# Kernel tuning notes

Measured on AMD Instinct MI355X. Metric: run time of the kernel, lower is better.

Reference implementation:

```python
import jax, jax.numpy as jnp
import numpy as np

IMAGE_SIZE = 512
OUT_SIZE = 64
FEAT = 256
SCALES = [2.0, 4.0, 6.0]
RATIOS = [0.5, 1.0, 2.0]
POS_THR = 0.7
NEG_THR = 0.3
HW = OUT_SIZE - 2            # head grid after 3x3 VALID conv
A = len(SCALES) * len(RATIOS)
B, N = 16, 8


def _anchor_base():
    # mirrors get_anchor_base(out_size-2, ratios, scales): w=scale*ratio, h=scale,
    # centers at i+0.5, boxes [xmin,ymin,xmax,ymax] clipped to [0, HW]
    ctr = np.arange(HW, dtype=np.float32) + 0.5
    ws = np.array([s * r for r in RATIOS for s in SCALES], np.float32)
    hs = np.array([s for r in RATIOS for s in SCALES], np.float32)
    X = ctr[:, None, None]  # x index first, as in the torch loop
    Y = ctr[None, :, None]
    xmin = np.clip(X - ws / 2, 0, HW)
    xmax = np.clip(X + ws / 2, 0, HW)
    ymin = np.clip(Y - hs / 2, 0, HW)
    ymax = np.clip(Y + hs / 2, 0, HW)
    xmin, ymin, xmax, ymax = np.broadcast_arrays(xmin, ymin, xmax, ymax)
    return np.stack([xmin, ymin, xmax, ymax], -1).reshape(-1, 4)  # [T,4]


def _conv(x, w, b):
    y = jax.lax.conv_general_dilated(x, w, (1, 1), 'VALID',
                                     dimension_numbers=('NCHW', 'OIHW', 'NCHW'))
    return y + b[None, :, None, None]


def setup_inputs() -> dict:
    key = jax.random.key(0)
    ks = jax.random.split(key, 8)
    features = jax.random.normal(ks[0], (B, FEAT, OUT_SIZE, OUT_SIZE), jnp.float32)
    cxy = jax.random.uniform(ks[1], (B, N, 2), jnp.float32, 0.0, IMAGE_SIZE)
    half = jax.random.uniform(ks[2], (B, N, 2), jnp.float32, 10.0, 60.0)
    mins = jnp.clip(cxy - half, 0.0, IMAGE_SIZE)
    maxs = jnp.clip(cxy + half, 0.0, IMAGE_SIZE)
    gt_boxes = jnp.concatenate([mins, maxs], -1)  # [B,N,4] xyxy in image coords
    gt_class = jax.random.randint(ks[3], (B, N), 0, 21)
    conv_w = jax.random.normal(ks[4], (FEAT, FEAT, 3, 3), jnp.float32) * 0.02
    conv_b = jnp.zeros((FEAT,), jnp.float32)
    cls_w = jax.random.normal(ks[5], (A, FEAT, 1, 1), jnp.float32) * 0.02
    cls_b = jnp.zeros((A,), jnp.float32)
    box_w = jax.random.normal(ks[6], (4 * A, FEAT, 1, 1), jnp.float32) * 0.02
    box_b = jnp.zeros((4 * A,), jnp.float32)
    return dict(features=features, gt_boxes=gt_boxes, gt_class=gt_class,
                conv_w=conv_w, conv_b=conv_b, cls_w=cls_w, cls_b=cls_b,
                box_w=box_w, box_b=box_b)


def reference(features, gt_boxes, gt_class, conv_w, conv_b, cls_w, cls_b, box_w, box_b):
    b = features.shape[0]
    x = _conv(features, conv_w, conv_b)          # [B,FEAT,HW,HW]
    cls = _conv(x, cls_w, cls_b)                 # [B,A,HW,HW]
    bx = _conv(x, box_w, box_b)                  # [B,4A,HW,HW]
    cls = cls.transpose(0, 2, 3, 1).reshape(b, -1)                    # [B,T]
    pred_off = bx.transpose(0, 2, 3, 1).reshape(b, -1, 4)             # [B,T,4]

    anchors = jnp.asarray(_anchor_base())        # [T,4]
    scale = IMAGE_SIZE // HW
    gt = gt_boxes / scale                        # project_bboxes p2a

    ax1, ay1, ax2, ay2 = (anchors[:, i] for i in range(4))
    gx1, gy1, gx2, gy2 = (gt[..., i] for i in range(4))
    area_a = (ax2 - ax1) * (ay2 - ay1)                                 # [T]
    area_g = (gx2 - gx1) * (gy2 - gy1)                                 # [B,N]
    ix1 = jnp.maximum(ax1[None, :, None], gx1[:, None, :])
    iy1 = jnp.maximum(ay1[None, :, None], gy1[:, None, :])
    ix2 = jnp.minimum(ax2[None, :, None], gx2[:, None, :])
    iy2 = jnp.minimum(ay2[None, :, None], gy2[:, None, :])
    inter = jnp.clip(ix2 - ix1, 0) * jnp.clip(iy2 - iy1, 0)            # [B,T,N]
    union = area_a[None, :, None] + area_g[:, None, :] - inter
    iou = inter / jnp.maximum(union, 1e-9)                             # [B,T,N]

    max_per_gt = iou.max(axis=1, keepdims=True)                        # best anchor per GT
    pos_mask = ((iou == max_per_gt) & (max_per_gt > 0)) | (iou > POS_THR)
    posf = pos_mask.astype(jnp.float32)
    num_pos = jnp.maximum(posf.sum(), 1.0)

    # anchor / gt boxes in cxcywh
    acx, acy = (ax1 + ax2) / 2, (ay1 + ay2) / 2
    aw, ah = ax2 - ax1, ay2 - ay1
    gcx, gcy = (gx1 + gx2) / 2, (gy1 + gy2) / 2
    gw, gh = gx2 - gx1, gy2 - gy1
    # per (anchor, gt) pair offsets [B,T,N,4]
    tx = (gcx[:, None, :] - acx[None, :, None]) / aw[None, :, None]
    ty = (gcy[:, None, :] - acy[None, :, None]) / ah[None, :, None]
    tw = jnp.log(gw)[:, None, :] - jnp.log(aw)[None, :, None]
    th = jnp.log(gh)[:, None, :] - jnp.log(ah)[None, :, None]
    gt_off = jnp.stack([tx, ty, tw, th], -1)

    diff = pred_off[:, :, None, :] - gt_off
    ad = jnp.abs(diff)
    sl1 = jnp.where(ad < 1.0, 0.5 * diff * diff, ad - 0.5)
    reg_loss = (sl1 * posf[..., None]).sum() / (num_pos * 4.0)

    # BCE-with-logits: positives target 1, negatives (iou < neg_thr) target 0
    pos_loss = (jax.nn.softplus(-cls)[:, :, None] * posf).sum() / num_pos
    negf = (iou < NEG_THR).astype(jnp.float32)
    num_neg = jnp.maximum(negf.sum(), 1.0)
    neg_loss = (jax.nn.softplus(cls)[:, :, None] * negf).sum() / num_neg
    cls_loss = 0.5 * (pos_loss + neg_loss)

    # proposals from predicted offsets, all anchors (positives selectable via pos_mask)
    pcx = acx[None, :] + pred_off[..., 0] * aw[None, :]
    pcy = acy[None, :] + pred_off[..., 1] * ah[None, :]
    pw = aw[None, :] * jnp.exp(pred_off[..., 2])
    ph = ah[None, :] * jnp.exp(pred_off[..., 3])
    proposal_scale = OUT_SIZE / HW
    proposals = jnp.stack([pcx - pw / 2, pcy - ph / 2, pcx + pw / 2, pcy + ph / 2],
                          -1) * proposal_scale                          # [B,T,4]

    # class of best-matching GT per anchor (GT_pos_class analogue, full grid)
    best_gt = jnp.argmax(iou, axis=-1)                                  # [B,T]
    gt_cls_per_anchor = jnp.take_along_axis(
        jnp.broadcast_to(gt_class[:, None, :], iou.shape).astype(jnp.int32),
        best_gt[..., None].astype(jnp.int32), -1)[..., 0]

    return (cls_loss, reg_loss, proposals, pos_mask, gt_cls_per_anchor)
```

## Files before the change

### kernel.cpp

```cpp
#include <hip/hip_runtime.h>
#include <math.h>

#define HW2   62
#define NANCH 34596
#define NBAT  16
#define NGT   8
#define FEATC 256
#define NOUT  45
#define NBLK_C 496

typedef short bf16x8 __attribute__((ext_vector_type(8)));
typedef float f32x4  __attribute__((ext_vector_type(4)));
typedef float f32x2  __attribute__((ext_vector_type(2)));

#define AS1U(p) ((const __attribute__((address_space(1))) unsigned int*)(p))
#define AS3U(p) ((__attribute__((address_space(3))) unsigned int*)(p))

__device__ __forceinline__ unsigned short f2bf(float f) {
    unsigned int u = __float_as_uint(f);
    u = u + 0x7FFFu + ((u >> 16) & 1u);
    return (unsigned short)(u >> 16);
}


__device__ __forceinline__ void anchor4(int i, int j, int a,
                                        float& x1, float& y1, float& x2, float& y2) {
    int am = a % 3, ad = a / 3;
    float h = 2.f * (float)(am + 1);
    float w = h * 0.5f * (float)(1 << ad);
    float cx = (float)i + 0.5f, cy = (float)j + 0.5f;
    x1 = fminf(fmaxf(cx - 0.5f * w, 0.f), 62.f);
    x2 = fminf(fmaxf(cx + 0.5f * w, 0.f), 62.f);
    y1 = fminf(fmaxf(cy - 0.5f * h, 0.f), 62.f);
    y2 = fminf(fmaxf(cy + 0.5f * h, 0.f), 62.f);
}

__device__ __forceinline__ float iou_fn(float ax1, float ay1, float ax2, float ay2,
                                        float gx1, float gy1, float gx2, float gy2) {
    float area_a = __fmul_rn(__fsub_rn(ax2, ax1), __fsub_rn(ay2, ay1));
    float area_g = __fmul_rn(__fsub_rn(gx2, gx1), __fsub_rn(gy2, gy1));
    float ix1 = fmaxf(ax1, gx1), iy1 = fmaxf(ay1, gy1);
    float ix2 = fminf(ax2, gx2), iy2 = fminf(ay2, gy2);
    float iw = fmaxf(__fsub_rn(ix2, ix1), 0.f);
    float ih = fmaxf(__fsub_rn(iy2, iy1), 0.f);
    float inter = __fmul_rn(iw, ih);
    float uni = __fsub_rn(__fadd_rn(area_a, area_g), inter);
    return inter / fmaxf(uni, 1e-9f);
}

__device__ __forceinline__ float softplus_f(float x) {
    return fmaxf(x, 0.f) + log1pf(expf(-fabsf(x)));
}

__device__ __forceinline__ float sl1_f(float d) {
    float ad = fabsf(d);
    return (ad < 1.f) ? 0.5f * d * d : (ad - 0.5f);
}

__device__ __forceinline__ void to_bf16_body(const float* __restrict__ feat,
                                             unsigned short* __restrict__ ft,
                                             float* ldsT,
                                             int yp, int cc, int bz, int b, int t) {
    int y0 = yp * 2;
#pragma unroll
    for (int k = 0; k < 4; ++k) {
        int fi = k * 256 + t;
        int ch = fi >> 5, r = fi & 31;
        int y = r >> 4, xq = r & 15;
        f32x4 v = *(const f32x4*)(feat + ((size_t)(b * 256 + cc * 32 + ch) << 12)
                                  + (y0 + y) * 64 + xq * 4);
        int word = ch * 128 + y * 64 + ((xq * 4) ^ ((ch & 7) << 3));
        *(f32x4*)(ldsT + word) = v;
    }
    __syncthreads();
    int y = t >> 7, x = (t >> 1) & 63, h2 = t & 1;
    bf16x8 o0, o1;
#pragma unroll
    for (int j = 0; j < 8; ++j) {
        int ch = h2 * 16 + j;
        o0[j] = (short)f2bf(ldsT[ch * 128 + y * 64 + (x ^ ((ch & 7) << 3))]);
    }
#pragma unroll
    for (int j = 0; j < 8; ++j) {
        int ch = h2 * 16 + 8 + j;
        o1[j] = (short)f2bf(ldsT[ch * 128 + y * 64 + (x ^ ((ch & 7) << 3))]);
    }
    unsigned short* ftc = ft + ((size_t)(bz * 8 + cc) << 17);
    size_t p = (size_t)(y0 + y) * 64 + x;
    *(bf16x8*)(ftc + ((size_t)(h2 * 2) * 4096 + p) * 8) = o0;
    *(bf16x8*)(ftc + ((size_t)(h2 * 2 + 1) * 4096 + p) * 8) = o1;
}

__global__ void prep_all(const float* __restrict__ feat,
                         const float* __restrict__ conv_w,
                         const float* __restrict__ conv_b,
                         const float* __restrict__ cls_w,
                         const float* __restrict__ cls_b,
                         const float* __restrict__ box_w,
                         const float* __restrict__ box_b,
                         const float* __restrict__ gtb,
                         unsigned short* __restrict__ Bfrag,
                         float* __restrict__ effb,
                         float* __restrict__ maxiou,
                         unsigned short* __restrict__ ft) {
    __shared__ float ldsT[4096];
    __shared__ float red[256];
    int blk = blockIdx.x, t = threadIdx.x;
    if (blk < 432) {
        int i = blk * 256 + t;
        int o = i / 2304, idx = i - o * 2304;
        float s = 0.f;
        if (o < NOUT) {
            const float* w2 = (o < 9) ? (cls_w + o * FEATC) : (box_w + (o - 9) * FEATC);
#pragma unroll 8
            for (int m = 0; m < FEATC; ++m)
                s = fmaf(w2[m], conv_w[(size_t)m * 2304 + idx], s);
        }
        int c = idx / 9, tap = idx - c * 9;
        size_t slot = (((size_t)(c >> 5) * 9 + tap) * 3 + (o >> 4)) * 512
                    + (size_t)((((c >> 3) & 3) * 16) + (o & 15)) * 8 + (c & 7);
        Bfrag[slot] = f2bf(s);
    } else if (blk < 560) {
        int bg = blk - 432;
        int b = bg >> 3, g = bg & 7;
        const float* p = gtb + (b * NGT + g) * 4;
        float gx1 = p[0] * 0.125f, gy1 = p[1] * 0.125f;
        float gx2 = p[2] * 0.125f, gy2 = p[3] * 0.125f;
        float m = 0.f;
        for (int n = t; n < NANCH; n += 256) {
            int i = n / 558; int r = n - i * 558; int j = r / 9; int a = r - j * 9;
            float ax1, ay1, ax2, ay2;
            anchor4(i, j, a, ax1, ay1, ax2, ay2);
            m = fmaxf(m, iou_fn(ax1, ay1, ax2, ay2, gx1, gy1, gx2, gy2));
        }
        red[t] = m;
        __syncthreads();
        for (int s = 128; s > 0; s >>= 1) {
            if (t < s) red[t] = fmaxf(red[t], red[t + s]);
            __syncthreads();
        }
        if (t == 0) maxiou[bg] = red[0];
    } else if (blk == 560) {
        if (t < 48) {
            float bv = 0.f;
            if (t < NOUT) {
                bv = (t < 9) ? cls_b[t] : box_b[t - 9];
                const float* w2 = (t < 9) ? (cls_w + t * FEATC) : (box_w + (t - 9) * FEATC);
                for (int mid = 0; mid < FEATC; ++mid) bv = fmaf(w2[mid], conv_b[mid], bv);
            }
            effb[t] = bv;
        }
    } else {
        int u = blk - 561;
        int yp = u & 31, cc = (u >> 5) & 7, bz = u >> 8;
        to_bf16_body(feat, ft, ldsT, yp, cc, bz, bz, t);
    }
}

__launch_bounds__(512, 4)
__global__ void conv_fused(const unsigned short* __restrict__ ft,
                           const unsigned short* __restrict__ Bfrag,
                           const float* __restrict__ effb,
                           const float* __restrict__ gtb,
                           const int* __restrict__ gtc,
                           const float* __restrict__ maxiou,
                           float* __restrict__ outp,
                           float* __restrict__ blksums) {
    __shared__ __align__(16) unsigned char Bs[2][27648];
    __shared__ float gshr[40];
    __shared__ float wred[8][5];

    float (*Cs)[49]  = (float (*)[49])&Bs[0][0];
    float (*Cs1)[49] = (float (*)[49])&Bs[1][0];

    const int t = threadIdx.x, l = t & 63, w = t >> 6;
    const int l15 = l & 15, lq = l >> 4;
    const int slot = w & 3, kg = w >> 2;

    int cpx = gridDim.x >> 3;
    int wgid = (blockIdx.x & 7) * cpx + (blockIdx.x >> 3);
    const int band = wgid % 31, b = wgid / 31;
    const int y0 = band * 2;

    if (t < 32) gshr[t] = gtb[b * 32 + t] * 0.125f;
    else if (t < 40) gshr[t] = maxiou[b * 8 + (t - 32)];

    f32x4 acc[2][3];
#pragma unroll
    for (int nf = 0; nf < 3; ++nf) {
        float bv = (kg == 0) ? effb[nf * 16 + l15] : 0.f;
#pragma unroll
        for (int mf = 0; mf < 2; ++mf)
#pragma unroll
            for (int r2 = 0; r2 < 4; ++r2) acc[mf][nf][r2] = bv;
    }

    int p0 = slot * 32 + l15;      if (p0 > 123) p0 = 123;
    int p1 = slot * 32 + 16 + l15; if (p1 > 123) p1 = 123;
    int rr0 = p0 / 62, c0 = p0 - rr0 * 62;
    int rr1 = p1 / 62, c1 = p1 - rr1 * 62;
    const int aoff0 = (lq << 12) + (y0 + rr0) * 64 + c0;
    const int aoff1 = (lq << 12) + (y0 + rr1) * 64 + c1;

    for (int i = 0; i < 4; ++i) {
#pragma unroll
        for (int k = 0; k < 7; ++k) {
            int u = t + k * 512;
            if (u < 3456) {
                int buf = (u >= 1728) ? 1 : 0;
                int idx = u - buf * 1728;
                int cs = buf ? (4 + i) : i;
                __builtin_amdgcn_global_load_lds(
                    AS1U(Bfrag + (size_t)cs * 13824 + (size_t)idx * 8),
                    AS3U(&Bs[buf][0] + idx * 16), 16, 0, 0);
            }
        }
        __syncthreads();

        int cc = kg * 4 + i;
        const unsigned short* ftc = ft + ((size_t)(b * 8 + cc) << 17);
        const unsigned char* Bb = &Bs[kg][0];
#pragma unroll
        for (int dy = 0; dy < 3; ++dy) {
            bf16x8 a0[3], a1[3];
#pragma unroll
            for (int dx = 0; dx < 3; ++dx) {
                int d = dy * 64 + dx;
                a0[dx] = *(const bf16x8*)(ftc + (size_t)(aoff0 + d) * 8);
                a1[dx] = *(const bf16x8*)(ftc + (size_t)(aoff1 + d) * 8);
            }
            __builtin_amdgcn_sched_barrier(0);
#pragma unroll
            for (int dx = 0; dx < 3; ++dx) {
                int tap = dy * 3 + dx;
#pragma unroll
                for (int nf = 0; nf < 3; ++nf) {
                    bf16x8 bfr = *(const bf16x8*)(Bb + (((tap * 3 + nf) << 6) + l) * 16);
                    acc[0][nf] = __builtin_amdgcn_mfma_f32_16x16x32_bf16(a0[dx], bfr, acc[0][nf], 0, 0, 0);
                    acc[1][nf] = __builtin_amdgcn_mfma_f32_16x16x32_bf16(a1[dx], bfr, acc[1][nf], 0, 0, 0);
                }
            }
        }
        __syncthreads();
    }

    {
        float (*Cdst)[49] = (kg == 0) ? Cs : Cs1;
#pragma unroll
        for (int mf = 0; mf < 2; ++mf)
#pragma unroll
            for (int nf = 0; nf < 3; ++nf)
#pragma unroll
                for (int r2 = 0; r2 < 4; ++r2) {
                    int pix = slot * 32 + mf * 16 + lq * 4 + r2;
                    if (pix < 124) Cdst[pix][nf * 16 + l15] = acc[mf][nf][r2];
                }
    }
    __syncthreads();

    float s_pos = 0.f, s_neg = 0.f, s_pl = 0.f, s_nl = 0.f, s_reg = 0.f;
    float* out_prop = outp + 2;
    float* out_mask = out_prop + (size_t)NBAT * NANCH * 4;
    float* out_gtc  = out_mask + (size_t)NBAT * NANCH * 8;

    for (int k = 0; k < 3; ++k) {
        int an = k * 512 + t;
        if (an < 1116) {
            int pixloc = an / 9, a = an - pixloc * 9;
            int rr = pixloc / 62, col = pixloc - rr * 62;
            int oy = y0 + rr, ox = col;
            int n = oy * 558 + ox * 9 + a;
            float cls = Cs[pixloc][a]          + Cs1[pixloc][a];
            float p0f = Cs[pixloc][9 + 4 * a]  + Cs1[pixloc][9 + 4 * a];
            float p1f = Cs[pixloc][10 + 4 * a] + Cs1[pixloc][10 + 4 * a];
            float p2f = Cs[pixloc][11 + 4 * a] + Cs1[pixloc][11 + 4 * a];
            float p3f = Cs[pixloc][12 + 4 * a] + Cs1[pixloc][12 + 4 * a];

            float ax1, ay1, ax2, ay2;
            anchor4(oy, ox, a, ax1, ay1, ax2, ay2);
            float aw = ax2 - ax1, ah = ay2 - ay1;
            float acx = 0.5f * (ax1 + ax2), acy = 0.5f * (ay1 + ay2);

            const float ps = 64.f / 62.f;
            float pcx = acx + p0f * aw, pcy = acy + p1f * ah;
            float pw = aw * expf(p2f), ph = ah * expf(p3f);
            float* pp = out_prop + ((size_t)b * NANCH + n) * 4;
            f32x2 pr0 = { (pcx - 0.5f * pw) * ps, (pcy - 0.5f * ph) * ps };
            f32x2 pr1 = { (pcx + 0.5f * pw) * ps, (pcy + 0.5f * ph) * ps };
            *(f32x2*)(pp) = pr0;
            *(f32x2*)(pp + 2) = pr1;

            float law = logf(aw), lah = logf(ah);
            float posf_tot = 0.f, negf_tot = 0.f;
            float best_iou = -1.f; int best_g = 0;
            float pfv[8];
#pragma unroll
            for (int g = 0; g < NGT; ++g) {
                float gx1 = gshr[g * 4 + 0], gy1 = gshr[g * 4 + 1];
                float gx2 = gshr[g * 4 + 2], gy2 = gshr[g * 4 + 3];
                float iou = iou_fn(ax1, ay1, ax2, ay2, gx1, gy1, gx2, gy2);
                float mpg = gshr[32 + g];
                bool pm = ((iou == mpg) && (mpg > 0.f)) || (iou > 0.7f);
                float pf = pm ? 1.f : 0.f;
                float nf = (iou < 0.3f) ? 1.f : 0.f;
                pfv[g] = pf;
                posf_tot += pf; negf_tot += nf;
                if (iou > best_iou) { best_iou = iou; best_g = g; }
                if (pm) {
                    float gw = gx2 - gx1, gh = gy2 - gy1;
                    float gcx = 0.5f * (gx1 + gx2), gcy = 0.5f * (gy1 + gy2);
                    float tx_ = (gcx - acx) / aw, ty_ = (gcy - acy) / ah;
                    float tw_ = logf(gw) - law, th_ = logf(gh) - lah;
                    float d0 = p0f - tx_, d1 = p1f - ty_, d2 = p2f - tw_, d3 = p3f - th_;
                    s_reg += sl1_f(d0) + sl1_f(d1) + sl1_f(d2) + sl1_f(d3);
                }
            }
            float* mp = out_mask + ((size_t)b * NANCH + n) * 8;
#pragma unroll
            for (int g = 0; g < 8; g += 2) {
                f32x2 mv = { pfv[g], pfv[g + 1] };
                *(f32x2*)(mp + g) = mv;
            }
            s_pos += posf_tot; s_neg += negf_tot;
            s_pl += softplus_f(-cls) * posf_tot;
            s_nl += softplus_f(cls) * negf_tot;
            out_gtc[(size_t)b * NANCH + n] = (float)gtc[b * NGT + best_g];
        }
    }

    int blk = b * 31 + band;
    float vals[5] = {s_pos, s_neg, s_pl, s_nl, s_reg};
#pragma unroll
    for (int s = 0; s < 5; ++s) {
        float v = vals[s];
#pragma unroll
        for (int m = 32; m >= 1; m >>= 1) v += __shfl_xor(v, m, 64);
        if (l == 0) wred[w][s] = v;
    }
    __syncthreads();
    if (t < 40) {
        int s = t >> 3, ww = t & 7;
        float v = wred[ww][s];
        v += __shfl_xor(v, 4, 64);
        v += __shfl_xor(v, 2, 64);
        v += __shfl_xor(v, 1, 64);
        if (ww == 0) blksums[(size_t)s * NBLK_C + blk] = v;
    }
}

__global__ void finalize(const float* __restrict__ blksums, float* __restrict__ outp) {
    __shared__ float red[256];
    __shared__ float tot[5];
    int t = threadIdx.x;
#pragma unroll
    for (int s = 0; s < 5; ++s) {
        float a = 0.f;
        for (int i = t; i < NBLK_C; i += 256) a += blksums[(size_t)s * NBLK_C + i];
        red[t] = a;
        __syncthreads();
        for (int st = 128; st > 0; st >>= 1) {
            if (t < st) red[t] += red[t + st];
            __syncthreads();
        }
        if (t == 0) tot[s] = red[0];
        __syncthreads();
    }
    if (t == 0) {
        float np_ = fmaxf(tot[0], 1.f), nn_ = fmaxf(tot[1], 1.f);
        outp[0] = 0.5f * (tot[2] / np_ + tot[3] / nn_);
        outp[1] = tot[4] / (np_ * 4.f);
    }
}

extern "C" void kernel_launch(void* const* d_in, const int* in_sizes, int n_in,
                              void* d_out, int out_size, void* d_ws, size_t ws_size,
                              hipStream_t stream) {
    (void)in_sizes; (void)n_in; (void)out_size; (void)ws_size;
    const float* feat   = (const float*)d_in[0];
    const float* gtb    = (const float*)d_in[1];
    const int*   gtc    = (const int*)d_in[2];
    const float* conv_w = (const float*)d_in[3];
    const float* conv_b = (const float*)d_in[4];
    const float* cls_w  = (const float*)d_in[5];
    const float* cls_b  = (const float*)d_in[6];
    const float* box_w  = (const float*)d_in[7];
    const float* box_b  = (const float*)d_in[8];
    float* outp = (float*)d_out;
    float* ws   = (float*)d_ws;

    unsigned short* Bfrag   = (unsigned short*)ws;
    float*          effb    = ws + 55296;
    float*          maxiou  = ws + 55360;
    float*          blksums = ws + 55488;
    unsigned short* ft      = (unsigned short*)(ws + 58048);

    prep_all<<<561 + 4096, 256, 0, stream>>>(feat, conv_w, conv_b, cls_w, cls_b,
                                             box_w, box_b, gtb, Bfrag, effb, maxiou, ft);
    conv_fused<<<NBLK_C, 512, 0, stream>>>(ft, Bfrag, effb, gtb, gtc, maxiou,
                                           outp, blksums);
    finalize<<<1, 256, 0, stream>>>(blksums, outp);
}
```

Before: 64.86 us.

## Fuse fp32-to-bf16 feature conversion into conv kernel loads

Drops the separate prep pass that transposed features into a channel-interleaved bf16 buffer. The conv kernel now reads fp32 features directly, doing eight strided scalar loads across channels and packing them with v_cvt_pk_bf16_f32. This removes a 4096-block transpose pass and the intermediate buffer round trip. In exchange the conv inner loop issues many uncoalesced scalar global loads and redundant reads across taps, where before it did single 16-byte loads.

Measured after the change: 111.4 us. +71.8%, slower.

```diff
diff --git a/kernel.cpp b/kernel.cpp
--- a/kernel.cpp
+++ b/kernel.cpp
@@ -20,6 +20,12 @@
     unsigned int u = __float_as_uint(f);
     u = u + 0x7FFFu + ((u >> 16) & 1u);
     return (unsigned short)(u >> 16);
+}
+
+__device__ __forceinline__ unsigned int pk_bf16(float lo, float hi) {
+    unsigned int r;
+    asm("v_cvt_pk_bf16_f32 %0, %1, %2" : "=v"(r) : "v"(lo), "v"(hi));
+    return r;
 }
 
 
@@ -57,42 +63,7 @@
     return (ad < 1.f) ? 0.5f * d * d : (ad - 0.5f);
 }
 
-__device__ __forceinline__ void to_bf16_body(const float* __restrict__ feat,
-                                             unsigned short* __restrict__ ft,
-                                             float* ldsT,
-                                             int yp, int cc, int bz, int b, int t) {
-    int y0 = yp * 2;
-#pragma unroll
-    for (int k = 0; k < 4; ++k) {
-        int fi = k * 256 + t;
-        int ch = fi >> 5, r = fi & 31;
-        int y = r >> 4, xq = r & 15;
-        f32x4 v = *(const f32x4*)(feat + ((size_t)(b * 256 + cc * 32 + ch) << 12)
-                                  + (y0 + y) * 64 + xq * 4);
-        int word = ch * 128 + y * 64 + ((xq * 4) ^ ((ch & 7) << 3));
-        *(f32x4*)(ldsT + word) = v;
-    }
-    __syncthreads();
-    int y = t >> 7, x = (t >> 1) & 63, h2 = t & 1;
-    bf16x8 o0, o1;
-#pragma unroll
-    for (int j = 0; j < 8; ++j) {
-        int ch = h2 * 16 + j;
-        o0[j] = (short)f2bf(ldsT[ch * 128 + y * 64 + (x ^ ((ch & 7) << 3))]);
-    }
-#pragma unroll
-    for (int j = 0; j < 8; ++j) {
-        int ch = h2 * 16 + 8 + j;
-        o1[j] = (short)f2bf(ldsT[ch * 128 + y * 64 + (x ^ ((ch & 7) << 3))]);
-    }
-    unsigned short* ftc = ft + ((size_t)(bz * 8 + cc) << 17);
-    size_t p = (size_t)(y0 + y) * 64 + x;
-    *(bf16x8*)(ftc + ((size_t)(h2 * 2) * 4096 + p) * 8) = o0;
-    *(bf16x8*)(ftc + ((size_t)(h2 * 2 + 1) * 4096 + p) * 8) = o1;
-}
-
-__global__ void prep_all(const float* __restrict__ feat,
-                         const float* __restrict__ conv_w,
+__global__ void prep_all(const float* __restrict__ conv_w,
                          const float* __restrict__ conv_b,
                          const float* __restrict__ cls_w,
                          const float* __restrict__ cls_b,
@@ -101,9 +72,7 @@
                          const float* __restrict__ gtb,
                          unsigned short* __restrict__ Bfrag,
                          float* __restrict__ effb,
-                         float* __restrict__ maxiou,
-                         unsigned short* __restrict__ ft) {
-    __shared__ float ldsT[4096];
+                         float* __restrict__ maxiou) {
     __shared__ float red[256];
     int blk = blockIdx.x, t = threadIdx.x;
     if (blk < 432) {
@@ -140,7 +109,7 @@
             __syncthreads();
         }
         if (t == 0) maxiou[bg] = red[0];
-    } else if (blk == 560) {
+    } else {
         if (t < 48) {
             float bv = 0.f;
             if (t < NOUT) {
@@ -150,15 +119,11 @@
             }
             effb[t] = bv;
         }
-    } else {
-        int u = blk - 561;
-        int yp = u & 31, cc = (u >> 5) & 7, bz = u >> 8;
-        to_bf16_body(feat, ft, ldsT, yp, cc, bz, bz, t);
     }
 }
 
 __launch_bounds__(512, 4)
-__global__ void conv_fused(const unsigned short* __restrict__ ft,
+__global__ void conv_fused(const float* __restrict__ feat,
                            const unsigned short* __restrict__ Bfrag,
                            const float* __restrict__ effb,
                            const float* __restrict__ gtb,
@@ -199,8 +164,18 @@
     int p1 = slot * 32 + 16 + l15; if (p1 > 123) p1 = 123;
     int rr0 = p0 / 62, c0 = p0 - rr0 * 62;
     int rr1 = p1 / 62, c1 = p1 - rr1 * 62;
-    const int aoff0 = (lq << 12) + (y0 + rr0) * 64 + c0;
-    const int aoff1 = (lq << 12) + (y0 + rr1) * 64 + c1;
+    const int abase0 = (y0 + rr0) * 64 + c0;
+    const int abase1 = (y0 + rr1) * 64 + c1;
+
+    auto load_pack = [&](const float* p) -> bf16x8 {
+        float v[8];
+#pragma unroll
+        for (int j = 0; j < 8; ++j) v[j] = p[(size_t)j << 12];
+        union { unsigned int u[4]; bf16x8 h; } r;
+#pragma unroll
+        for (int j = 0; j < 4; ++j) r.u[j] = pk_bf16(v[2 * j], v[2 * j + 1]);
+        return r.h;
+    };
 
     for (int i = 0; i < 4; ++i) {
 #pragma unroll
@@ -218,16 +193,17 @@
         __syncthreads();
 
         int cc = kg * 4 + i;
-        const unsigned short* ftc = ft + ((size_t)(b * 8 + cc) << 17);
+        const float* fc = feat + (((size_t)(b * 256 + cc * 32 + lq * 8)) << 12);
         const unsigned char* Bb = &Bs[kg][0];
 #pragma unroll
         for (int dy = 0; dy < 3; ++dy) {
+            const float* f0 = fc + abase0 + dy * 64;
+            const float* f1 = fc + abase1 + dy * 64;
             bf16x8 a0[3], a1[3];
 #pragma unroll
             for (int dx = 0; dx < 3; ++dx) {
-                int d = dy * 64 + dx;
-                a0[dx] = *(const bf16x8*)(ftc + (size_t)(aoff0 + d) * 8);
-                a1[dx] = *(const bf16x8*)(ftc + (size_t)(aoff1 + d) * 8);
+                a0[dx] = load_pack(f0 + dx);
+                a1[dx] = load_pack(f1 + dx);
             }
             __builtin_amdgcn_sched_barrier(0);
 #pragma unroll
@@ -392,11 +368,10 @@
     float*          effb    = ws + 55296;
     float*          maxiou  = ws + 55360;
     float*          blksums = ws + 55488;
-    unsigned short* ft      = (unsigned short*)(ws + 58048);
-
-    prep_all<<<561 + 4096, 256, 0, stream>>>(feat, conv_w, conv_b, cls_w, cls_b,
-                                             box_w, box_b, gtb, Bfrag, effb, maxiou, ft);
-    conv_fused<<<NBLK_C, 512, 0, stream>>>(ft, Bfrag, effb, gtb, gtc, maxiou,
+
+    prep_all<<<561, 256, 0, stream>>>(conv_w, conv_b, cls_w, cls_b,
+                                      box_w, box_b, gtb, Bfrag, effb, maxiou);
+    conv_fused<<<NBLK_C, 512, 0, stream>>>(feat, Bfrag, effb, gtb, gtc, maxiou,
                                            outp, blksums);
     finalize<<<1, 256, 0, stream>>>(blksums, outp);
 }
```
